# Performance work log

Measured on AMD Instinct MI355X. Metric: run time of the kernel, lower is better.

The kernel has to match this reference:

```python
import jax, jax.numpy as jnp
import numpy as np
from jax import lax

B, S, H = 64, 128, 64
EPS = 1e-5


def _conv1d(x, w, b):
    # x: [B, Cin, S], w: [Cout, Cin, 3], padding=1
    y = lax.conv_general_dilated(x, w, window_strides=(1,), padding=[(1, 1)],
                                 dimension_numbers=("NCH", "OIH", "NCH"))
    return y + b[None, :, None]


def _bn(x, g, b, m, v):
    # eval-mode BatchNorm1d over channel dim of [B, C, S]
    inv = g / jnp.sqrt(v + EPS)
    return x * inv[None, :, None] + (b - m * inv)[None, :, None]


def setup_inputs() -> dict:
    key = jax.random.key(0)
    ks = jax.random.split(key, 24)
    d = {}
    d["x"] = jax.random.normal(ks[0], (B, S, 1), dtype=jnp.float32)
    sc = 0.1
    d["conv1_w"] = jax.random.normal(ks[1], (H, 1, 3), dtype=jnp.float32) * sc
    d["conv1_b"] = jax.random.normal(ks[2], (H,), dtype=jnp.float32) * sc
    d["bn1_g"] = jax.random.uniform(ks[3], (H,), dtype=jnp.float32) + 0.5
    d["bn1_b"] = jax.random.normal(ks[4], (H,), dtype=jnp.float32) * sc
    d["bn1_m"] = jax.random.normal(ks[5], (H,), dtype=jnp.float32) * sc
    d["bn1_v"] = jax.random.uniform(ks[6], (H,), dtype=jnp.float32) + 0.5
    d["conv2_w"] = jax.random.normal(ks[7], (H, H, 3), dtype=jnp.float32) * 0.05
    d["conv2_b"] = jax.random.normal(ks[8], (H,), dtype=jnp.float32) * sc
    d["bn2_g"] = jax.random.uniform(ks[9], (H,), dtype=jnp.float32) + 0.5
    d["bn2_b"] = jax.random.normal(ks[10], (H,), dtype=jnp.float32) * sc
    d["bn2_m"] = jax.random.normal(ks[11], (H,), dtype=jnp.float32) * sc
    d["bn2_v"] = jax.random.uniform(ks[12], (H,), dtype=jnp.float32) + 0.5
    d["gat_W"] = jax.random.normal(ks[13], (H, H), dtype=jnp.float32) * 0.05
    d["gat_Wb"] = jax.random.normal(ks[14], (H,), dtype=jnp.float32) * sc
    d["gat_a1"] = jax.random.normal(ks[15], (H,), dtype=jnp.float32) * sc
    d["gat_a2"] = jax.random.normal(ks[16], (H,), dtype=jnp.float32) * sc
    d["gat_ab"] = jax.random.normal(ks[17], (), dtype=jnp.float32) * sc
    d["ta_W"] = jax.random.normal(ks[18], (H, H), dtype=jnp.float32) * 0.05
    d["ta_b"] = jax.random.normal(ks[19], (H,), dtype=jnp.float32) * sc
    d["p1_W"] = jax.random.normal(ks[20], (32, H), dtype=jnp.float32) * sc
    d["p1_b"] = jax.random.normal(ks[21], (32,), dtype=jnp.float32) * sc
    d["p2_W"] = jax.random.normal(ks[22], (1, 32), dtype=jnp.float32) * sc
    d["p2_b"] = jax.random.normal(ks[23], (1,), dtype=jnp.float32) * sc
    return d


def reference(x, conv1_w, conv1_b, bn1_g, bn1_b, bn1_m, bn1_v,
              conv2_w, conv2_b, bn2_g, bn2_b, bn2_m, bn2_v,
              gat_W, gat_Wb, gat_a1, gat_a2, gat_ab,
              ta_W, ta_b, p1_W, p1_b, p2_W, p2_b):
    b, s, _ = x.shape
    # feature extraction: [B, 1, S] -> [B, H, S]
    h = jnp.transpose(x, (0, 2, 1))
    h = jax.nn.relu(_bn(_conv1d(h, conv1_w, conv1_b), bn1_g, bn1_b, bn1_m, bn1_v))
    h = jax.nn.relu(_bn(_conv1d(h, conv2_w, conv2_b), bn2_g, bn2_b, bn2_m, bn2_v))
    # flatten to N = B*S nodes of dim H
    xf = jnp.transpose(h, (0, 2, 1)).reshape(b * s, H)  # [N, H]
    # dense adjacency: softmax(xf xf^T) over rows (single chunk since B<=100)
    adj = jax.nn.softmax(xf @ xf.T, axis=1)  # [N, N]
    # GAT layer; pairwise score decomposed: a([Wh_i;Wh_j]) = Wh_i.a1 + Wh_j.a2 + b
    Wh = xf @ gat_W.T + gat_Wb  # [N, H]
    s1 = Wh @ gat_a1  # [N]
    s2 = Wh @ gat_a2  # [N]
    e = jax.nn.leaky_relu(s1[:, None] + s2[None, :] + gat_ab, 0.2)  # [N, N]
    e = jnp.where(adj > 0, e, jnp.float32(-9e15))
    att = jax.nn.softmax(e, axis=1)
    hp = att @ Wh  # [N, H]
    h2 = hp.reshape(b, s, H)
    # time attention over feature dim
    tw = jax.nn.softmax(h2 @ ta_W.T + ta_b, axis=2)
    h2 = h2 * tw
    # global average pool over sequence
    pooled = jnp.mean(h2, axis=1)  # [B, H]
    out = jax.nn.relu(pooled @ p1_W.T + p1_b) @ p2_W.T + p2_b  # [B, 1]
    return out
```

## Files before the change

kernel.cpp:

```cpp
#include <hip/hip_runtime.h>
#include <hip/hip_bf16.h>

#define Hd 64
#define Sd 128
#define Bd 64
#define Nn 8192
#define EPSd 1e-5f

__device__ __forceinline__ float wred_sum(float v) {
    for (int m = 32; m; m >>= 1) v += __shfl_xor(v, m);
    return v;
}
__device__ __forceinline__ float wred_max(float v) {
    for (int m = 32; m; m >>= 1) v = fmaxf(v, __shfl_xor(v, m));
    return v;
}
__device__ __forceinline__ float wscan_incl(float x, int lane) {
    #pragma unroll
    for (int d = 1; d < 64; d <<= 1) {
        float t = __shfl_up(x, d);
        if (lane >= d) x += t;
    }
    return x;
}

__global__ __launch_bounds__(256) void kA_feat_wh(
        const float* __restrict__ x,
        const float* __restrict__ c1w, const float* __restrict__ c1b,
        const float* __restrict__ b1g, const float* __restrict__ b1b,
        const float* __restrict__ b1m, const float* __restrict__ b1v,
        const float* __restrict__ c2w, const float* __restrict__ c2b,
        const float* __restrict__ b2g, const float* __restrict__ b2b,
        const float* __restrict__ b2m, const float* __restrict__ b2v,
        const float* __restrict__ gW, const float* __restrict__ gWb,
        const float* __restrict__ a1, const float* __restrict__ a2,
        float* __restrict__ Wh, float* __restrict__ s1, float* __restrict__ s2) {
    __shared__ float buf[14464];
    float* h1  = buf;
    float* wtk = buf + 2176;
    int b  = blockIdx.x >> 2;
    int s0 = (blockIdx.x & 3) * 32;
    int tid = threadIdx.x;
    for (int idx = tid; idx < 12288; idx += 256) {
        int c   = idx / 192;
        int rem = idx - c * 192;
        int cin = rem / 3;
        int k   = rem - cin * 3;
        int cin4 = cin >> 2, j = cin & 3;
        wtk[(k * 16 + cin4) * 256 + c * 4 + j] = c2w[idx];
    }
    for (int idx = tid; idx < 34 * 64; idx += 256) {
        int cin = idx & 63;
        int col = idx >> 6;
        int s   = s0 - 1 + col;
        float v = 0.f;
        if (s >= 0 && s < Sd) {
            float xm = (s > 0)      ? x[b * Sd + s - 1] : 0.f;
            float x0 = x[b * Sd + s];
            float xp = (s < Sd - 1) ? x[b * Sd + s + 1] : 0.f;
            float y  = c1w[cin * 3 + 0] * xm + c1w[cin * 3 + 1] * x0 + c1w[cin * 3 + 2] * xp + c1b[cin];
            float inv = b1g[cin] * rsqrtf(b1v[cin] + EPSd);
            v = fmaxf(y * inv + (b1b[cin] - b1m[cin] * inv), 0.f);
        }
        h1[col * 64 + cin] = v;
    }
    __syncthreads();
    int c = tid & 63, g = tid >> 6;
    float inv2 = b2g[c] * rsqrtf(b2v[c] + EPSd);
    float sh2  = b2b[c] - b2m[c] * inv2;
    float acc[8];
    #pragma unroll
    for (int p = 0; p < 8; ++p) acc[p] = c2b[c];
    {
        const float4* h14 = (const float4*)h1;
        const float4* wt4 = (const float4*)wtk;
        for (int cin4 = 0; cin4 < 16; ++cin4) {
            float4 xs[10];
            #pragma unroll
            for (int q = 0; q < 10; ++q) xs[q] = h14[(g * 8 + q) * 16 + cin4];
            #pragma unroll
            for (int k = 0; k < 3; ++k) {
                float4 w4 = wt4[(k * 16 + cin4) * 64 + c];
                #pragma unroll
                for (int p = 0; p < 8; ++p) {
                    float4 x4 = xs[p + k];
                    acc[p] += w4.x * x4.x + w4.y * x4.y + w4.z * x4.z + w4.w * x4.w;
                }
            }
        }
    }
    __syncthreads();
    float*  xfl  = buf;
    float4* gWT4 = (float4*)(buf + 2176);
    #pragma unroll
    for (int p = 0; p < 8; ++p)
        xfl[(g * 8 + p) * 64 + c] = fmaxf(acc[p] * inv2 + sh2, 0.f);
    for (int fidx = tid; fidx < 1024; fidx += 256) {
        int h_ = fidx >> 4, kk4 = fidx & 15;
        gWT4[kk4 * 64 + h_] = ((const float4*)gW)[fidx];
    }
    __syncthreads();
    int h = tid & 63, w = tid >> 6;
    float4 wreg[16];
    #pragma unroll
    for (int kk4 = 0; kk4 < 16; ++kk4) wreg[kk4] = gWT4[kk4 * 64 + h];
    float va1 = a1[h], va2 = a2[h], bias = gWb[h];
    const float4* xf4 = (const float4*)xfl;
    int n0 = b * Sd + s0;
    for (int q = 0; q < 8; ++q) {
        int sl = w * 8 + q;
        float accw = bias;
        #pragma unroll
        for (int kk4 = 0; kk4 < 16; ++kk4) {
            float4 x4 = xf4[sl * 16 + kk4];
            accw += wreg[kk4].x * x4.x + wreg[kk4].y * x4.y + wreg[kk4].z * x4.z + wreg[kk4].w * x4.w;
        }
        int n = n0 + sl;
        Wh[n * 64 + h] = accw;
        float r1 = wred_sum(accw * va1);
        float r2 = wred_sum(accw * va2);
        if (h == 0) { s1[n] = r1; s2[n] = r2; }
    }
}

__global__ __launch_bounds__(256) void kB_rank(
        const float* __restrict__ s2, const float* __restrict__ s1,
        const float* __restrict__ gab,
        int* __restrict__ rankPart, int* __restrict__ kPart,
        float* __restrict__ pmax) {
    __shared__ float4 ts4[64];
    int bid = blockIdx.x;
    int jg = bid >> 5, part = bid & 31;
    int tid = threadIdx.x;
    if (tid < 64) ts4[tid] = ((const float4*)(s2 + part * 256))[tid];
    __syncthreads();
    if (jg == 0 && tid < 64) {
        float4 t4 = ts4[tid];
        float m = fmaxf(fmaxf(t4.x, t4.y), fmaxf(t4.z, t4.w));
        m = wred_max(m);
        if (tid == 0) pmax[part] = m;
    }
    int j = jg * 256 + tid;
    float tj = s2[j];
    float negc = -(s1[j] + gab[0]);
    int jloc = j - part * 256;
    int cntR = 0, cntK = 0;
    #pragma unroll 4
    for (int q = 0; q < 64; ++q) {
        float4 t4 = ts4[q];
        int rb = q * 4;
        cntR += (t4.x < tj || (t4.x == tj && rb     < jloc)) ? 1 : 0;
        cntR += (t4.y < tj || (t4.y == tj && rb + 1 < jloc)) ? 1 : 0;
        cntR += (t4.z < tj || (t4.z == tj && rb + 2 < jloc)) ? 1 : 0;
        cntR += (t4.w < tj || (t4.w == tj && rb + 3 < jloc)) ? 1 : 0;
        cntK += (t4.x <= negc) ? 1 : 0;
        cntK += (t4.y <= negc) ? 1 : 0;
        cntK += (t4.z <= negc) ? 1 : 0;
        cntK += (t4.w <= negc) ? 1 : 0;
    }
    rankPart[part * 8192 + j] = cntR;
    kPart[part * 8192 + j]    = cntK;
}

__global__ __launch_bounds__(256) void kC_scatter(
        const float* __restrict__ s2,
        const int* __restrict__ rankPart, const int* __restrict__ kPart,
        int* __restrict__ jsorted, float* __restrict__ e1so, float* __restrict__ e2so,
        int* __restrict__ kk) {
    int j = blockIdx.x * 256 + threadIdx.x;
    int r = 0, kq = 0;
    #pragma unroll
    for (int p = 0; p < 32; ++p) { r += rankPart[p * 8192 + j]; kq += kPart[p * 8192 + j]; }
    float t = s2[j];
    jsorted[r] = j;
    e1so[r] = expf(t);
    e2so[r] = expf(0.2f * t);
    kk[j] = kq;
}

__global__ __launch_bounds__(256) void kD_dual(
        const float* __restrict__ Wh, const int* __restrict__ jsorted,
        const float* __restrict__ e1so, const float* __restrict__ e2so,
        float* __restrict__ csP, float* __restrict__ csN,
        float* __restrict__ csp, float* __restrict__ csn,
        float* __restrict__ PLpos, float* __restrict__ PLneg,
        float* __restrict__ pLp, float* __restrict__ pLn) {
    __shared__ float ldsA[4][64], ldsB[4][64];
    int bid = blockIdx.x, tid = threadIdx.x;
    int h = tid & 63, w = tid >> 6;
    if (bid < 64) {
        int ch = bid;
        int rb = ch * 128 + w * 32;
        double aP = 0.0, aN = 0.0;
        #pragma unroll
        for (int r = 0; r < 32; ++r) {
            int j = jsorted[rb + r];
            float wv = Wh[j * 64 + h];
            aP += e1so[rb + r] * wv;
            aN += e2so[rb + r] * wv;
        }
        ldsA[w][h] = (float)aP; ldsB[w][h] = (float)aN;
        __syncthreads();
        if (w == 0) {
            csP[ch * 64 + h] = ldsA[0][h] + ldsA[1][h] + ldsA[2][h] + ldsA[3][h];
        } else if (w == 1) {
            csN[ch * 64 + h] = ldsB[0][h] + ldsB[1][h] + ldsB[2][h] + ldsB[3][h];
        } else if (w == 2) {
            float vv = e1so[ch * 128 + h] + e1so[ch * 128 + 64 + h];
            vv = wred_sum(vv);
            if (h == 0) csp[ch] = vv;
        } else {
            float vv = e2so[ch * 128 + h] + e2so[ch * 128 + 64 + h];
            vv = wred_sum(vv);
            if (h == 0) csn[ch] = vv;
        }
    } else {
        int ch = bid - 64;
        int rb = ch * 128 + w * 32;
        float v[32], u[32];
        #pragma unroll
        for (int r = 0; r < 32; ++r) {
            int j = jsorted[rb + r];
            float wv = Wh[j * 64 + h];
            v[r] = e1so[rb + r] * wv;
            u[r] = e2so[rb + r] * wv;
        }
        double sP = 0.0, sN = 0.0;
        #pragma unroll
        for (int r = 0; r < 32; ++r) { sP += v[r]; sN += u[r]; }
        ldsA[w][h] = (float)sP; ldsB[w][h] = (float)sN;
        __syncthreads();
        float offP = 0.f, offN = 0.f;
        #pragma unroll
        for (int w2 = 0; w2 < 4; ++w2) if (w2 < w) { offP += ldsA[w2][h]; offN += ldsB[w2][h]; }
        double a = 0.0;
        #pragma unroll
        for (int r = 0; r < 32; ++r) { PLpos[(rb + r) * 64 + h] = offP + (float)a; a += v[r]; }
        a = 0.0;
        #pragma unroll
        for (int r = 0; r < 32; ++r) { PLneg[(rb + r) * 64 + h] = offN + (float)a; a += u[r]; }
        if (w == 0) {
            int lane = h;
            float v0 = e1so[ch * 128 + lane], v1 = e1so[ch * 128 + 64 + lane];
            float i0 = wscan_incl(v0, lane);
            float t0 = __shfl(i0, 63);
            float i1 = wscan_incl(v1, lane);
            pLp[ch * 128 + lane]      = i0 - v0;
            pLp[ch * 128 + 64 + lane] = t0 + i1 - v1;
        } else if (w == 1) {
            int lane = h;
            float v0 = e2so[ch * 128 + lane], v1 = e2so[ch * 128 + 64 + lane];
            float i0 = wscan_incl(v0, lane);
            float t0 = __shfl(i0, 63);
            float i1 = wscan_incl(v1, lane);
            pLn[ch * 128 + lane]      = i0 - v0;
            pLn[ch * 128 + 64 + lane] = t0 + i1 - v1;
        }
    }
}

__global__ __launch_bounds__(256) void kF_node(
        const float* __restrict__ s1, const int* __restrict__ kk,
        const float* __restrict__ pmax, const float* __restrict__ gab,
        const float* __restrict__ PLpos, const float* __restrict__ PLneg,
        const float* __restrict__ pLp, const float* __restrict__ pLn,
        const float* __restrict__ csP, const float* __restrict__ csN,
        const float* __restrict__ csp, const float* __restrict__ csn,
        const float* __restrict__ taW, const float* __restrict__ tab,
        float* __restrict__ h2) {
    __shared__ float4 wt4[1024];
    __shared__ float hl[16 * 64];
    __shared__ float cpP[65 * 64], cpN[65 * 64];
    __shared__ float cpp[65], cpn[65];
    int tid = threadIdx.x;
    int h = tid & 63, w = tid >> 6;
    for (int fidx = tid; fidx < 1024; fidx += 256) {
        int h_ = fidx >> 4, kk4 = fidx & 15;
        wt4[kk4 * 64 + h_] = ((const float4*)taW)[fidx];
    }
    if (w == 0) {
        double a = 0.0;
        for (int ch = 0; ch < 64; ++ch) { cpP[ch * 64 + h] = (float)a; a += csP[ch * 64 + h]; }
        cpP[64 * 64 + h] = (float)a;
    } else if (w == 1) {
        double a = 0.0;
        for (int ch = 0; ch < 64; ++ch) { cpN[ch * 64 + h] = (float)a; a += csN[ch * 64 + h]; }
        cpN[64 * 64 + h] = (float)a;
    } else if (w == 2) {
        float v = csp[h];
        float i = wscan_incl(v, h);
        cpp[h] = i - v;
        if (h == 63) cpp[64] = i;
    } else {
        float v = csn[h];
        float i = wscan_incl(v, h);
        cpn[h] = i - v;
        if (h == 63) cpn[64] = i;
    }
    float tmx = pmax[tid & 31];
    tmx = wred_max(tmx);
    __syncthreads();
    float gabv = gab[0];
    float tabv = tab[h];
    float Tp  = cpP[64 * 64 + h];
    float ppT = cpp[64];
    for (int r = 0; r < 4; ++r) {
        int n = blockIdx.x * 16 + w * 4 + r;
        float c = s1[n] + gabv;
        int k = kk[n];
        int ch = k >> 7;
        float PLpv = 0.f, PLnv = 0.f, pLpv = 0.f, pLnv = 0.f;
        if (k < Nn) {
            PLpv = PLpos[k * 64 + h]; PLnv = PLneg[k * 64 + h];
            pLpv = pLp[k];            pLnv = pLn[k];
        }
        float Pp = cpP[ch * 64 + h] + PLpv;
        float Pn = cpN[ch * 64 + h] + PLnv;
        float qp = cpp[ch] + pLpv;
        float qn = cpn[ch] + pLnv;
        float z = c + tmx;
        float m = (z >= 0.f) ? z : 0.2f * z;
        float E1 = expf(c - m), E2 = expf(0.2f * c - m);
        float num = E1 * (Tp - Pp) + E2 * Pn;
        float den = E1 * (ppT - qp) + E2 * qn;
        float hp = num / den;
        int slot = w * 4 + r;
        hl[slot * 64 + h] = hp;
        float vv = tabv;
        const float4* hlr = (const float4*)&hl[slot * 64];
        #pragma unroll
        for (int kk4 = 0; kk4 < 16; ++kk4) {
            float4 w4 = wt4[kk4 * 64 + h];
            float4 x4 = hlr[kk4];
            vv += w4.x * x4.x + w4.y * x4.y + w4.z * x4.z + w4.w * x4.w;
        }
        float mx = wred_max(vv);
        float e = expf(vv - mx);
        float se = wred_sum(e);
        h2[n * 64 + h] = hp * (e / se);
    }
}

__global__ __launch_bounds__(256) void kG_pool(
        const float* __restrict__ h2,
        const float* __restrict__ p1W, const float* __restrict__ p1b,
        const float* __restrict__ p2W, const float* __restrict__ p2b,
        float* __restrict__ out) {
    __shared__ float pacc[4 * 64];
    __shared__ float pl[64];
    __shared__ float p1s[32 * 65];
    int tid = threadIdx.x, b = blockIdx.x;
    int w = tid >> 6, h = tid & 63;
    for (int idx = tid; idx < 2048; idx += 256) {
        int q = idx >> 6, kq = idx & 63;
        p1s[q * 65 + kq] = p1W[idx];
    }
    float a = 0.f;
    for (int s = w * 32; s < w * 32 + 32; ++s) a += h2[(b * Sd + s) * 64 + h];
    pacc[w * 64 + h] = a;
    __syncthreads();
    if (w == 0) {
        float pooled = (pacc[h] + pacc[64 + h] + pacc[128 + h] + pacc[192 + h]) * (1.f / 128.f);
        pl[h] = pooled;
        float val = 0.f;
        if (h < 32) {
            float acc = p1b[h];
            #pragma unroll
            for (int kq = 0; kq < 64; ++kq) acc += p1s[h * 65 + kq] * pl[kq];
            val = p2W[h] * fmaxf(acc, 0.f);
        }
        val = wred_sum(val);
        if (h == 0) out[b] = val + p2b[0];
    }
}

extern "C" void kernel_launch(void* const* d_in, const int* in_sizes, int n_in,
                              void* d_out, int out_size, void* d_ws, size_t ws_size,
                              hipStream_t stream) {
    const float* x    = (const float*)d_in[0];
    const float* c1w  = (const float*)d_in[1];
    const float* c1b  = (const float*)d_in[2];
    const float* b1g  = (const float*)d_in[3];
    const float* b1b  = (const float*)d_in[4];
    const float* b1m  = (const float*)d_in[5];
    const float* b1v  = (const float*)d_in[6];
    const float* c2w  = (const float*)d_in[7];
    const float* c2b  = (const float*)d_in[8];
    const float* b2g  = (const float*)d_in[9];
    const float* b2b  = (const float*)d_in[10];
    const float* b2m  = (const float*)d_in[11];
    const float* b2v  = (const float*)d_in[12];
    const float* gW   = (const float*)d_in[13];
    const float* gWb  = (const float*)d_in[14];
    const float* ga1  = (const float*)d_in[15];
    const float* ga2  = (const float*)d_in[16];
    const float* gab  = (const float*)d_in[17];
    const float* taW  = (const float*)d_in[18];
    const float* tab  = (const float*)d_in[19];
    const float* p1W  = (const float*)d_in[20];
    const float* p1b  = (const float*)d_in[21];
    const float* p2W  = (const float*)d_in[22];
    const float* p2b  = (const float*)d_in[23];
    float* out = (float*)d_out;

    float* ws = (float*)d_ws;
    float* Wh      = ws;
    float* s1      = Wh + 524288;
    float* s2v     = s1 + 8192;
    float* e1so    = s2v + 8192;
    float* e2so    = e1so + 8192;
    float* csP     = e2so + 8192;
    float* csN     = csP + 4096;
    float* csp     = csN + 4096;
    float* csn     = csp + 64;
    float* pmax    = csn + 64;
    float* pLp     = pmax + 64;
    float* pLn     = pLp + 8192;
    float* PLpos   = pLn + 8192;
    float* PLneg   = PLpos + 524288;
    int*   jsorted = (int*)(PLneg + 524288);
    int*   kk      = jsorted + 8192;
    int*   rankPart= kk + 8192;
    int*   kPart   = rankPart + 262144;
    float* h2      = (float*)rankPart;

    kA_feat_wh<<<256, 256, 0, stream>>>(x, c1w, c1b, b1g, b1b, b1m, b1v,
                                        c2w, c2b, b2g, b2b, b2m, b2v,
                                        gW, gWb, ga1, ga2, Wh, s1, s2v);
    kB_rank<<<1024, 256, 0, stream>>>(s2v, s1, gab, rankPart, kPart, pmax);
    kC_scatter<<<32, 256, 0, stream>>>(s2v, rankPart, kPart, jsorted, e1so, e2so, kk);
    kD_dual<<<128, 256, 0, stream>>>(Wh, jsorted, e1so, e2so, csP, csN, csp, csn,
                                     PLpos, PLneg, pLp, pLn);
    kF_node<<<512, 256, 0, stream>>>(s1, kk, pmax, gab, PLpos, PLneg, pLp, pLn,
                                     csP, csN, csp, csn, taW, tab, h2);
    kG_pool<<<64, 256, 0, stream>>>(h2, p1W, p1b, p2W, p2b, out);
}
```

Measured before the change: 58.86 us.

## Fuse rank+scatter into one kernel and fuse node attention with pooling

Merges the partial-rank and scatter kernels into one kernel. Each block loads all 8192 keys into LDS and computes full ranks for 16 nodes, reducing across 16 slices in shared memory, so the rankPart/kPart global round trip goes away. Also fuses the per-node time-attention kernel with the average pool and MLP head: one 1024-thread block per batch accumulates pooled sums in registers instead of writing h2 to global memory. This cuts two launches and the intermediate traffic, but leaves only 64 blocks for the fused node kernel and puts a large LDS footprint on the rank kernel.

```diff
diff --git a/kernel.cpp b/kernel.cpp
--- a/kernel.cpp
+++ b/kernel.cpp
@@ -123,59 +123,57 @@
     }
 }
 
-__global__ __launch_bounds__(256) void kB_rank(
+__global__ __launch_bounds__(256) void kBC_rank(
         const float* __restrict__ s2, const float* __restrict__ s1,
         const float* __restrict__ gab,
-        int* __restrict__ rankPart, int* __restrict__ kPart,
-        float* __restrict__ pmax) {
-    __shared__ float4 ts4[64];
-    int bid = blockIdx.x;
-    int jg = bid >> 5, part = bid & 31;
-    int tid = threadIdx.x;
-    if (tid < 64) ts4[tid] = ((const float4*)(s2 + part * 256))[tid];
-    __syncthreads();
-    if (jg == 0 && tid < 64) {
-        float4 t4 = ts4[tid];
-        float m = fmaxf(fmaxf(t4.x, t4.y), fmaxf(t4.z, t4.w));
+        int* __restrict__ jsorted, float* __restrict__ e1so, float* __restrict__ e2so,
+        int* __restrict__ kk, float* __restrict__ pmax) {
+    __shared__ float keys[8192];
+    __shared__ int rcnt[16][16], kcnt[16][16];
+    int tid = threadIdx.x, bid = blockIdx.x;
+    for (int i = tid; i < 2048; i += 256)
+        ((float4*)keys)[i] = ((const float4*)s2)[i];
+    __syncthreads();
+    if (bid == 0) {
+        float m = -1e30f;
+        for (int i = tid; i < 8192; i += 256) m = fmaxf(m, keys[i]);
         m = wred_max(m);
-        if (tid == 0) pmax[part] = m;
-    }
-    int j = jg * 256 + tid;
-    float tj = s2[j];
+        if ((tid & 63) == 0) pmax[tid >> 6] = m;
+    }
+    int jj = tid & 15, slice = tid >> 4;
+    int j = bid * 16 + jj;
+    float tj = keys[j];
     float negc = -(s1[j] + gab[0]);
-    int jloc = j - part * 256;
     int cntR = 0, cntK = 0;
+    const float4* k4 = (const float4*)keys;
+    int qbase = slice * 128;
     #pragma unroll 4
-    for (int q = 0; q < 64; ++q) {
-        float4 t4 = ts4[q];
-        int rb = q * 4;
-        cntR += (t4.x < tj || (t4.x == tj && rb     < jloc)) ? 1 : 0;
-        cntR += (t4.y < tj || (t4.y == tj && rb + 1 < jloc)) ? 1 : 0;
-        cntR += (t4.z < tj || (t4.z == tj && rb + 2 < jloc)) ? 1 : 0;
-        cntR += (t4.w < tj || (t4.w == tj && rb + 3 < jloc)) ? 1 : 0;
+    for (int q = 0; q < 128; ++q) {
+        int qi = qbase + ((q + slice) & 127);
+        float4 t4 = k4[qi];
+        int kidx = qi * 4;
+        cntR += (t4.x < tj || (t4.x == tj && kidx     < j)) ? 1 : 0;
+        cntR += (t4.y < tj || (t4.y == tj && kidx + 1 < j)) ? 1 : 0;
+        cntR += (t4.z < tj || (t4.z == tj && kidx + 2 < j)) ? 1 : 0;
+        cntR += (t4.w < tj || (t4.w == tj && kidx + 3 < j)) ? 1 : 0;
         cntK += (t4.x <= negc) ? 1 : 0;
         cntK += (t4.y <= negc) ? 1 : 0;
         cntK += (t4.z <= negc) ? 1 : 0;
         cntK += (t4.w <= negc) ? 1 : 0;
     }
-    rankPart[part * 8192 + j] = cntR;
-    kPart[part * 8192 + j]    = cntK;
-}
-
-__global__ __launch_bounds__(256) void kC_scatter(
-        const float* __restrict__ s2,
-        const int* __restrict__ rankPart, const int* __restrict__ kPart,
-        int* __restrict__ jsorted, float* __restrict__ e1so, float* __restrict__ e2so,
-        int* __restrict__ kk) {
-    int j = blockIdx.x * 256 + threadIdx.x;
-    int r = 0, kq = 0;
-    #pragma unroll
-    for (int p = 0; p < 32; ++p) { r += rankPart[p * 8192 + j]; kq += kPart[p * 8192 + j]; }
-    float t = s2[j];
-    jsorted[r] = j;
-    e1so[r] = expf(t);
-    e2so[r] = expf(0.2f * t);
-    kk[j] = kq;
+    rcnt[slice][jj] = cntR; kcnt[slice][jj] = cntK;
+    __syncthreads();
+    if (tid < 16) {
+        int r = 0, kq = 0;
+        #pragma unroll
+        for (int s_ = 0; s_ < 16; ++s_) { r += rcnt[s_][tid]; kq += kcnt[s_][tid]; }
+        int jg = bid * 16 + tid;
+        float t = keys[jg];
+        jsorted[r] = jg;
+        e1so[r] = expf(t);
+        e2so[r] = expf(0.2f * t);
+        kk[jg] = kq;
+    }
 }
 
 __global__ __launch_bounds__(256) void kD_dual(
@@ -259,7 +257,7 @@
     }
 }
 
-__global__ __launch_bounds__(256) void kF_node(
+__global__ __launch_bounds__(1024) void kFG(
         const float* __restrict__ s1, const int* __restrict__ kk,
         const float* __restrict__ pmax, const float* __restrict__ gab,
         const float* __restrict__ PLpos, const float* __restrict__ PLneg,
@@ -267,17 +265,18 @@
         const float* __restrict__ csP, const float* __restrict__ csN,
         const float* __restrict__ csp, const float* __restrict__ csn,
         const float* __restrict__ taW, const float* __restrict__ tab,
-        float* __restrict__ h2) {
+        const float* __restrict__ p1W, const float* __restrict__ p1b,
+        const float* __restrict__ p2W, const float* __restrict__ p2b,
+        float* __restrict__ out) {
     __shared__ float4 wt4[1024];
-    __shared__ float hl[16 * 64];
     __shared__ float cpP[65 * 64], cpN[65 * 64];
     __shared__ float cpp[65], cpn[65];
-    int tid = threadIdx.x;
+    __shared__ float hl[16 * 64];
+    __shared__ float pacc[16 * 64];
+    __shared__ float pl[64];
+    int tid = threadIdx.x, b = blockIdx.x;
     int h = tid & 63, w = tid >> 6;
-    for (int fidx = tid; fidx < 1024; fidx += 256) {
-        int h_ = fidx >> 4, kk4 = fidx & 15;
-        wt4[kk4 * 64 + h_] = ((const float4*)taW)[fidx];
-    }
+    wt4[(tid & 15) * 64 + (tid >> 4)] = ((const float4*)taW)[tid];
     if (w == 0) {
         double a = 0.0;
         for (int ch = 0; ch < 64; ++ch) { cpP[ch * 64 + h] = (float)a; a += csP[ch * 64 + h]; }
@@ -291,21 +290,21 @@
         float i = wscan_incl(v, h);
         cpp[h] = i - v;
         if (h == 63) cpp[64] = i;
-    } else {
+    } else if (w == 3) {
         float v = csn[h];
         float i = wscan_incl(v, h);
         cpn[h] = i - v;
         if (h == 63) cpn[64] = i;
     }
-    float tmx = pmax[tid & 31];
-    tmx = wred_max(tmx);
+    float tmx = fmaxf(fmaxf(pmax[0], pmax[1]), fmaxf(pmax[2], pmax[3]));
     __syncthreads();
     float gabv = gab[0];
     float tabv = tab[h];
     float Tp  = cpP[64 * 64 + h];
     float ppT = cpp[64];
-    for (int r = 0; r < 4; ++r) {
-        int n = blockIdx.x * 16 + w * 4 + r;
+    float apool = 0.f;
+    for (int q = 0; q < 8; ++q) {
+        int n = b * Sd + w * 8 + q;
         float c = s1[n] + gabv;
         int k = kk[n];
         int ch = k >> 7;
@@ -324,10 +323,9 @@
         float num = E1 * (Tp - Pp) + E2 * Pn;
         float den = E1 * (ppT - qp) + E2 * qn;
         float hp = num / den;
-        int slot = w * 4 + r;
-        hl[slot * 64 + h] = hp;
+        hl[w * 64 + h] = hp;
         float vv = tabv;
-        const float4* hlr = (const float4*)&hl[slot * 64];
+        const float4* hlr = (const float4*)&hl[w * 64];
         #pragma unroll
         for (int kk4 = 0; kk4 < 16; ++kk4) {
             float4 w4 = wt4[kk4 * 64 + h];
@@ -337,30 +335,25 @@
         float mx = wred_max(vv);
         float e = expf(vv - mx);
         float se = wred_sum(e);
-        h2[n * 64 + h] = hp * (e / se);
-    }
-}
-
-__global__ __launch_bounds__(256) void kG_pool(
-        const float* __restrict__ h2,
-        const float* __restrict__ p1W, const float* __restrict__ p1b,
-        const float* __restrict__ p2W, const float* __restrict__ p2b,
-        float* __restrict__ out) {
-    __shared__ float pacc[4 * 64];
-    __shared__ float pl[64];
-    __shared__ float p1s[32 * 65];
-    int tid = threadIdx.x, b = blockIdx.x;
-    int w = tid >> 6, h = tid & 63;
-    for (int idx = tid; idx < 2048; idx += 256) {
-        int q = idx >> 6, kq = idx & 63;
-        p1s[q * 65 + kq] = p1W[idx];
-    }
-    float a = 0.f;
-    for (int s = w * 32; s < w * 32 + 32; ++s) a += h2[(b * Sd + s) * 64 + h];
-    pacc[w * 64 + h] = a;
+        apool += hp * (e / se);
+    }
+    pacc[w * 64 + h] = apool;
+    __syncthreads();
+    float* p1s = (float*)wt4;
+    {
+        int idx = tid;
+        int q0 = idx >> 6, k0 = idx & 63;
+        p1s[q0 * 65 + k0] = p1W[idx];
+        idx += 1024;
+        int q1 = idx >> 6, k1 = idx & 63;
+        p1s[q1 * 65 + k1] = p1W[idx];
+    }
     __syncthreads();
     if (w == 0) {
-        float pooled = (pacc[h] + pacc[64 + h] + pacc[128 + h] + pacc[192 + h]) * (1.f / 128.f);
+        float pooled = 0.f;
+        #pragma unroll
+        for (int w2 = 0; w2 < 16; ++w2) pooled += pacc[w2 * 64 + h];
+        pooled *= (1.f / 128.f);
         pl[h] = pooled;
         float val = 0.f;
         if (h < 32) {
@@ -420,18 +413,14 @@
     float* PLneg   = PLpos + 524288;
     int*   jsorted = (int*)(PLneg + 524288);
     int*   kk      = jsorted + 8192;
-    int*   rankPart= kk + 8192;
-    int*   kPart   = rankPart + 262144;
-    float* h2      = (float*)rankPart;
 
     kA_feat_wh<<<256, 256, 0, stream>>>(x, c1w, c1b, b1g, b1b, b1m, b1v,
                                         c2w, c2b, b2g, b2b, b2m, b2v,
                                         gW, gWb, ga1, ga2, Wh, s1, s2v);
-    kB_rank<<<1024, 256, 0, stream>>>(s2v, s1, gab, rankPart, kPart, pmax);
-    kC_scatter<<<32, 256, 0, stream>>>(s2v, rankPart, kPart, jsorted, e1so, e2so, kk);
+    kBC_rank<<<512, 256, 0, stream>>>(s2v, s1, gab, jsorted, e1so, e2so, kk, pmax);
     kD_dual<<<128, 256, 0, stream>>>(Wh, jsorted, e1so, e2so, csP, csN, csp, csn,
                                      PLpos, PLneg, pLp, pLn);
-    kF_node<<<512, 256, 0, stream>>>(s1, kk, pmax, gab, PLpos, PLneg, pLp, pLn,
-                                     csP, csN, csp, csn, taW, tab, h2);
-    kG_pool<<<64, 256, 0, stream>>>(h2, p1W, p1b, p2W, p2b, out);
-}
+    kFG<<<64, 1024, 0, stream>>>(s1, kk, pmax, gab, PLpos, PLneg, pLp, pLn,
+                                 csP, csN, csp, csn, taW, tab,
+                                 p1W, p1b, p2W, p2b, out);
+}
```

Measured after the change: 85.48 us. 1.45x slower.

## Fuse per-node attention kernel with pooling head into one per-batch kernel

Applied to the files above, without the earlier changes.

Merges the node-output kernel and the pooling/MLP head into a single kernel with one 1024-thread block per batch. Each block handles that batch's 128 nodes and accumulates the pooled sum in registers and shared memory, so the [N,H] h2 intermediate is never written to or read back from global memory and one launch is dropped. In exchange the grid shrinks from 512 blocks to 64 large blocks, which may leave many compute units idle. Each block also redoes the prefix setup (cpP/cpN scans, ta_W transpose), now serialized over fewer blocks.

```diff
diff --git a/kernel.cpp b/kernel.cpp
--- a/kernel.cpp
+++ b/kernel.cpp
@@ -259,7 +259,7 @@
     }
 }
 
-__global__ __launch_bounds__(256) void kF_node(
+__global__ __launch_bounds__(1024) void kFG(
         const float* __restrict__ s1, const int* __restrict__ kk,
         const float* __restrict__ pmax, const float* __restrict__ gab,
         const float* __restrict__ PLpos, const float* __restrict__ PLneg,
@@ -267,17 +267,18 @@
         const float* __restrict__ csP, const float* __restrict__ csN,
         const float* __restrict__ csp, const float* __restrict__ csn,
         const float* __restrict__ taW, const float* __restrict__ tab,
-        float* __restrict__ h2) {
+        const float* __restrict__ p1W, const float* __restrict__ p1b,
+        const float* __restrict__ p2W, const float* __restrict__ p2b,
+        float* __restrict__ out) {
     __shared__ float4 wt4[1024];
-    __shared__ float hl[16 * 64];
     __shared__ float cpP[65 * 64], cpN[65 * 64];
     __shared__ float cpp[65], cpn[65];
-    int tid = threadIdx.x;
+    __shared__ float hl[16 * 64];
+    __shared__ float pacc[16 * 64];
+    __shared__ float pl[64];
+    int tid = threadIdx.x, b = blockIdx.x;
     int h = tid & 63, w = tid >> 6;
-    for (int fidx = tid; fidx < 1024; fidx += 256) {
-        int h_ = fidx >> 4, kk4 = fidx & 15;
-        wt4[kk4 * 64 + h_] = ((const float4*)taW)[fidx];
-    }
+    wt4[(tid & 15) * 64 + (tid >> 4)] = ((const float4*)taW)[tid];
     if (w == 0) {
         double a = 0.0;
         for (int ch = 0; ch < 64; ++ch) { cpP[ch * 64 + h] = (float)a; a += csP[ch * 64 + h]; }
@@ -291,7 +292,7 @@
         float i = wscan_incl(v, h);
         cpp[h] = i - v;
         if (h == 63) cpp[64] = i;
-    } else {
+    } else if (w == 3) {
         float v = csn[h];
         float i = wscan_incl(v, h);
         cpn[h] = i - v;
@@ -304,8 +305,9 @@
     float tabv = tab[h];
     float Tp  = cpP[64 * 64 + h];
     float ppT = cpp[64];
-    for (int r = 0; r < 4; ++r) {
-        int n = blockIdx.x * 16 + w * 4 + r;
+    float apool = 0.f;
+    for (int q = 0; q < 8; ++q) {
+        int n = b * Sd + w * 8 + q;
         float c = s1[n] + gabv;
         int k = kk[n];
         int ch = k >> 7;
@@ -324,10 +326,9 @@
         float num = E1 * (Tp - Pp) + E2 * Pn;
         float den = E1 * (ppT - qp) + E2 * qn;
         float hp = num / den;
-        int slot = w * 4 + r;
-        hl[slot * 64 + h] = hp;
+        hl[w * 64 + h] = hp;
         float vv = tabv;
-        const float4* hlr = (const float4*)&hl[slot * 64];
+        const float4* hlr = (const float4*)&hl[w * 64];
         #pragma unroll
         for (int kk4 = 0; kk4 < 16; ++kk4) {
             float4 w4 = wt4[kk4 * 64 + h];
@@ -337,30 +338,25 @@
         float mx = wred_max(vv);
         float e = expf(vv - mx);
         float se = wred_sum(e);
-        h2[n * 64 + h] = hp * (e / se);
-    }
-}
-
-__global__ __launch_bounds__(256) void kG_pool(
-        const float* __restrict__ h2,
-        const float* __restrict__ p1W, const float* __restrict__ p1b,
-        const float* __restrict__ p2W, const float* __restrict__ p2b,
-        float* __restrict__ out) {
-    __shared__ float pacc[4 * 64];
-    __shared__ float pl[64];
-    __shared__ float p1s[32 * 65];
-    int tid = threadIdx.x, b = blockIdx.x;
-    int w = tid >> 6, h = tid & 63;
-    for (int idx = tid; idx < 2048; idx += 256) {
-        int q = idx >> 6, kq = idx & 63;
-        p1s[q * 65 + kq] = p1W[idx];
-    }
-    float a = 0.f;
-    for (int s = w * 32; s < w * 32 + 32; ++s) a += h2[(b * Sd + s) * 64 + h];
-    pacc[w * 64 + h] = a;
+        apool += hp * (e / se);
+    }
+    pacc[w * 64 + h] = apool;
+    __syncthreads();
+    float* p1s = (float*)wt4;
+    {
+        int idx = tid;
+        int q0 = idx >> 6, k0 = idx & 63;
+        p1s[q0 * 65 + k0] = p1W[idx];
+        idx += 1024;
+        int q1 = idx >> 6, k1 = idx & 63;
+        p1s[q1 * 65 + k1] = p1W[idx];
+    }
     __syncthreads();
     if (w == 0) {
-        float pooled = (pacc[h] + pacc[64 + h] + pacc[128 + h] + pacc[192 + h]) * (1.f / 128.f);
+        float pooled = 0.f;
+        #pragma unroll
+        for (int w2 = 0; w2 < 16; ++w2) pooled += pacc[w2 * 64 + h];
+        pooled *= (1.f / 128.f);
         pl[h] = pooled;
         float val = 0.f;
         if (h < 32) {
@@ -422,7 +418,6 @@
     int*   kk      = jsorted + 8192;
     int*   rankPart= kk + 8192;
     int*   kPart   = rankPart + 262144;
-    float* h2      = (float*)rankPart;
 
     kA_feat_wh<<<256, 256, 0, stream>>>(x, c1w, c1b, b1g, b1b, b1m, b1v,
                                         c2w, c2b, b2g, b2b, b2m, b2v,
@@ -431,7 +426,7 @@
     kC_scatter<<<32, 256, 0, stream>>>(s2v, rankPart, kPart, jsorted, e1so, e2so, kk);
     kD_dual<<<128, 256, 0, stream>>>(Wh, jsorted, e1so, e2so, csP, csN, csp, csn,
                                      PLpos, PLneg, pLp, pLn);
-    kF_node<<<512, 256, 0, stream>>>(s1, kk, pmax, gab, PLpos, PLneg, pLp, pLn,
-                                     csP, csN, csp, csn, taW, tab, h2);
-    kG_pool<<<64, 256, 0, stream>>>(h2, p1W, p1b, p2W, p2b, out);
-}
+    kFG<<<64, 1024, 0, stream>>>(s1, kk, pmax, gab, PLpos, PLneg, pLp, pLn,
+                                 csP, csN, csp, csn, taW, tab,
+                                 p1W, p1b, p2W, p2b, out);
+}
```

New measurement: 62.76 us. 6.6% more time.

## Fuse per-block pooling into node kernel and parallelize chunk prefix scans

Applied to the files above, without the earlier changes.

The node kernel now sums its weighted node outputs into per-block pooled partials instead of writing the full h2 tensor. The pool kernel then reads only 8 partial rows per batch, removing a large global write and re-read. The per-block chunk prefix sums, previously a serial 64-step double-precision loop in two waves, become wave-level float scans spread across all four waves, stored in padded shared arrays. Dropping from double to float accumulation in the scan may change numerics slightly.

```diff
diff --git a/kernel.cpp b/kernel.cpp
--- a/kernel.cpp
+++ b/kernel.cpp
@@ -267,45 +267,52 @@
         const float* __restrict__ csP, const float* __restrict__ csN,
         const float* __restrict__ csp, const float* __restrict__ csn,
         const float* __restrict__ taW, const float* __restrict__ tab,
-        float* __restrict__ h2) {
+        float* __restrict__ pp) {
     __shared__ float4 wt4[1024];
-    __shared__ float hl[16 * 64];
-    __shared__ float cpP[65 * 64], cpN[65 * 64];
-    __shared__ float cpp[65], cpn[65];
-    int tid = threadIdx.x;
+    __shared__ float cpP[65 * 65], cpN[65 * 65];
+    __shared__ float cpps[65], cpns[65];
+    __shared__ float hl[4][64];
+    __shared__ float pacc[4][64];
+    int tid = threadIdx.x, bid = blockIdx.x;
     int h = tid & 63, w = tid >> 6;
+    int lane = h;
     for (int fidx = tid; fidx < 1024; fidx += 256) {
         int h_ = fidx >> 4, kk4 = fidx & 15;
         wt4[kk4 * 64 + h_] = ((const float4*)taW)[fidx];
     }
-    if (w == 0) {
-        double a = 0.0;
-        for (int ch = 0; ch < 64; ++ch) { cpP[ch * 64 + h] = (float)a; a += csP[ch * 64 + h]; }
-        cpP[64 * 64 + h] = (float)a;
-    } else if (w == 1) {
-        double a = 0.0;
-        for (int ch = 0; ch < 64; ++ch) { cpN[ch * 64 + h] = (float)a; a += csN[ch * 64 + h]; }
-        cpN[64 * 64 + h] = (float)a;
-    } else if (w == 2) {
-        float v = csp[h];
-        float i = wscan_incl(v, h);
-        cpp[h] = i - v;
-        if (h == 63) cpp[64] = i;
-    } else {
-        float v = csn[h];
-        float i = wscan_incl(v, h);
-        cpn[h] = i - v;
-        if (h == 63) cpn[64] = i;
+    #pragma unroll
+    for (int rep = 0; rep < 16; ++rep) {
+        int hh = w * 16 + rep;
+        float v = csP[lane * 64 + hh];
+        float i = wscan_incl(v, lane);
+        cpP[lane * 65 + hh] = i - v;
+        if (lane == 63) cpP[64 * 65 + hh] = i;
+        float v2 = csN[lane * 64 + hh];
+        float i2 = wscan_incl(v2, lane);
+        cpN[lane * 65 + hh] = i2 - v2;
+        if (lane == 63) cpN[64 * 65 + hh] = i2;
+    }
+    if (w == 2) {
+        float v = csp[lane];
+        float i = wscan_incl(v, lane);
+        cpps[lane] = i - v;
+        if (lane == 63) cpps[64] = i;
+    } else if (w == 3) {
+        float v = csn[lane];
+        float i = wscan_incl(v, lane);
+        cpns[lane] = i - v;
+        if (lane == 63) cpns[64] = i;
     }
     float tmx = pmax[tid & 31];
     tmx = wred_max(tmx);
     __syncthreads();
     float gabv = gab[0];
     float tabv = tab[h];
-    float Tp  = cpP[64 * 64 + h];
-    float ppT = cpp[64];
+    float Tp  = cpP[64 * 65 + h];
+    float ppT = cpps[64];
+    float apool = 0.f;
     for (int r = 0; r < 4; ++r) {
-        int n = blockIdx.x * 16 + w * 4 + r;
+        int n = bid * 16 + w * 4 + r;
         float c = s1[n] + gabv;
         int k = kk[n];
         int ch = k >> 7;
@@ -314,20 +321,19 @@
             PLpv = PLpos[k * 64 + h]; PLnv = PLneg[k * 64 + h];
             pLpv = pLp[k];            pLnv = pLn[k];
         }
-        float Pp = cpP[ch * 64 + h] + PLpv;
-        float Pn = cpN[ch * 64 + h] + PLnv;
-        float qp = cpp[ch] + pLpv;
-        float qn = cpn[ch] + pLnv;
+        float Pp = cpP[ch * 65 + h] + PLpv;
+        float Pn = cpN[ch * 65 + h] + PLnv;
+        float qp = cpps[ch] + pLpv;
+        float qn = cpns[ch] + pLnv;
         float z = c + tmx;
         float m = (z >= 0.f) ? z : 0.2f * z;
         float E1 = expf(c - m), E2 = expf(0.2f * c - m);
         float num = E1 * (Tp - Pp) + E2 * Pn;
         float den = E1 * (ppT - qp) + E2 * qn;
         float hp = num / den;
-        int slot = w * 4 + r;
-        hl[slot * 64 + h] = hp;
+        hl[w][h] = hp;
         float vv = tabv;
-        const float4* hlr = (const float4*)&hl[slot * 64];
+        const float4* hlr = (const float4*)&hl[w][0];
         #pragma unroll
         for (int kk4 = 0; kk4 < 16; ++kk4) {
             float4 w4 = wt4[kk4 * 64 + h];
@@ -337,16 +343,20 @@
         float mx = wred_max(vv);
         float e = expf(vv - mx);
         float se = wred_sum(e);
-        h2[n * 64 + h] = hp * (e / se);
-    }
+        apool += hp * (e / se);
+    }
+    pacc[w][h] = apool;
+    __syncthreads();
+    if (w == 0)
+        pp[bid * 64 + h] = pacc[0][h] + pacc[1][h] + pacc[2][h] + pacc[3][h];
 }
 
 __global__ __launch_bounds__(256) void kG_pool(
-        const float* __restrict__ h2,
+        const float* __restrict__ pp,
         const float* __restrict__ p1W, const float* __restrict__ p1b,
         const float* __restrict__ p2W, const float* __restrict__ p2b,
         float* __restrict__ out) {
-    __shared__ float pacc[4 * 64];
+    __shared__ float pacc[4][64];
     __shared__ float pl[64];
     __shared__ float p1s[32 * 65];
     int tid = threadIdx.x, b = blockIdx.x;
@@ -355,12 +365,11 @@
         int q = idx >> 6, kq = idx & 63;
         p1s[q * 65 + kq] = p1W[idx];
     }
-    float a = 0.f;
-    for (int s = w * 32; s < w * 32 + 32; ++s) a += h2[(b * Sd + s) * 64 + h];
-    pacc[w * 64 + h] = a;
+    float a = pp[(b * 8 + w) * 64 + h] + pp[(b * 8 + 4 + w) * 64 + h];
+    pacc[w][h] = a;
     __syncthreads();
     if (w == 0) {
-        float pooled = (pacc[h] + pacc[64 + h] + pacc[128 + h] + pacc[192 + h]) * (1.f / 128.f);
+        float pooled = (pacc[0][h] + pacc[1][h] + pacc[2][h] + pacc[3][h]) * (1.f / 128.f);
         pl[h] = pooled;
         float val = 0.f;
         if (h < 32) {
@@ -416,13 +425,13 @@
     float* pmax    = csn + 64;
     float* pLp     = pmax + 64;
     float* pLn     = pLp + 8192;
-    float* PLpos   = pLn + 8192;
+    float* ppool   = pLn + 8192;
+    float* PLpos   = ppool + 32768;
     float* PLneg   = PLpos + 524288;
     int*   jsorted = (int*)(PLneg + 524288);
     int*   kk      = jsorted + 8192;
     int*   rankPart= kk + 8192;
     int*   kPart   = rankPart + 262144;
-    float* h2      = (float*)rankPart;
 
     kA_feat_wh<<<256, 256, 0, stream>>>(x, c1w, c1b, b1g, b1b, b1m, b1v,
                                         c2w, c2b, b2g, b2b, b2m, b2v,
@@ -432,6 +441,6 @@
     kD_dual<<<128, 256, 0, stream>>>(Wh, jsorted, e1so, e2so, csP, csN, csp, csn,
                                      PLpos, PLneg, pLp, pLn);
     kF_node<<<512, 256, 0, stream>>>(s1, kk, pmax, gab, PLpos, PLneg, pLp, pLn,
-                                     csP, csN, csp, csn, taW, tab, h2);
-    kG_pool<<<64, 256, 0, stream>>>(h2, p1W, p1b, p2W, p2b, out);
-}
+                                     csP, csN, csp, csn, taW, tab, ppool);
+    kG_pool<<<64, 256, 0, stream>>>(ppool, p1W, p1b, p2W, p2b, out);
+}
```

Result: slower. 67.14 us (+14.1%).
